# Performance work log

Measured on AMD Instinct MI355X. Metric: run time of the kernel, lower is better.

The kernel has to match this reference:

```python
import jax, jax.numpy as jnp
import numpy as np

LR, HR, H, D1 = 512, 2048, 4, 200
N = 2 * HR            # 4096 nodes (fully connected graph)
C1 = D1 // H          # 50  per-head dim, layer 1
C2 = HR // H          # 512 per-head dim, layer 2
EPS = 1e-5


def setup_inputs() -> dict:
    key = jax.random.key(0)
    ks = jax.random.split(key, 24)
    lin = lambda k, fi, fo: jax.random.normal(k, (fi, fo), jnp.float32) * 0.02
    vec = lambda k, d: jax.random.normal(k, (d,), jnp.float32) * 0.02
    inp = {"lr_x": jax.random.normal(ks[0], (LR, N), jnp.float32)}
    # TransformerConv 1: lr -> 200 (query/key/value/skip linears, each with bias)
    inp["Wq1"], inp["bq1"] = lin(ks[1], LR, D1), vec(ks[2], D1)
    inp["Wk1"], inp["bk1"] = lin(ks[3], LR, D1), vec(ks[4], D1)
    inp["Wv1"], inp["bv1"] = lin(ks[5], LR, D1), vec(ks[6], D1)
    inp["Ws1"], inp["bs1"] = lin(ks[7], LR, D1), vec(ks[8], D1)
    # GraphNorm 1
    inp["gn1_w"] = 1.0 + 0.1 * jax.random.normal(ks[9], (D1,), jnp.float32)
    inp["gn1_b"] = vec(ks[10], D1)
    inp["gn1_ms"] = 1.0 + 0.1 * jax.random.normal(ks[11], (D1,), jnp.float32)
    # TransformerConv 2: 200 -> 2048
    inp["Wq2"], inp["bq2"] = lin(ks[12], D1, HR), vec(ks[13], HR)
    inp["Wk2"], inp["bk2"] = lin(ks[14], D1, HR), vec(ks[15], HR)
    inp["Wv2"], inp["bv2"] = lin(ks[16], D1, HR), vec(ks[17], HR)
    inp["Ws2"], inp["bs2"] = lin(ks[18], D1, HR), vec(ks[19], HR)
    # GraphNorm 2
    inp["gn2_w"] = 1.0 + 0.1 * jax.random.normal(ks[20], (HR,), jnp.float32)
    inp["gn2_b"] = vec(ks[21], HR)
    inp["gn2_ms"] = 1.0 + 0.1 * jax.random.normal(ks[22], (HR,), jnp.float32)
    return inp


def _transformer_conv(x, Wq, bq, Wk, bk, Wv, bv, Ws, bs, heads, ch):
    # PyG TransformerConv on a fully-connected edge_index == dense multi-head attention
    n = x.shape[0]
    q = (x @ Wq + bq).reshape(n, heads, ch)
    k = (x @ Wk + bk).reshape(n, heads, ch)
    v = (x @ Wv + bv).reshape(n, heads, ch)
    scores = jnp.einsum('ihc,jhc->hij', q, k) / (ch ** 0.5)  # [H, N, N]
    attn = jax.nn.softmax(scores, axis=-1)                   # softmax over source nodes j
    out = jnp.einsum('hij,jhc->ihc', attn, v).reshape(n, heads * ch)
    return out + x @ Ws + bs                                 # root/skip connection


def _graph_norm(x, w, b, ms):
    # PyG GraphNorm: y = w * (x - ms*mean) / sqrt(E[(x - ms*mean)^2] + eps) + b
    mean = jnp.mean(x, axis=0, keepdims=True)
    out = x - mean * ms
    var = jnp.mean(out * out, axis=0, keepdims=True)
    return out * jax.lax.rsqrt(var + EPS) * w + b


def reference(lr_x, Wq1, bq1, Wk1, bk1, Wv1, bv1, Ws1, bs1, gn1_w, gn1_b, gn1_ms,
              Wq2, bq2, Wk2, bk2, Wv2, bv2, Ws2, bs2, gn2_w, gn2_b, gn2_ms):
    h = _transformer_conv(lr_x.T, Wq1, bq1, Wk1, bk1, Wv1, bv1, Ws1, bs1, H, C1)  # [N, 200]
    h = _graph_norm(h, gn1_w, gn1_b, gn1_ms)
    h2 = _transformer_conv(h, Wq2, bq2, Wk2, bk2, Wv2, bv2, Ws2, bs2, H, C2)      # [N, HR]
    h2 = _graph_norm(h2, gn2_w, gn2_b, gn2_ms).T                                  # [HR, N]
    h2 = h2 / jnp.linalg.norm(h2, axis=1, keepdims=True)
    return jax.nn.relu(h2 @ h2.T)                                                 # [HR, HR]
```

## Files before the change

### kernel.cpp

```cpp
#include <hip/hip_runtime.h>
#include <math.h>

typedef unsigned int u32;
typedef unsigned short ushort_t;
typedef __attribute__((ext_vector_type(8))) short short8;
typedef __attribute__((ext_vector_type(4))) float f32x4;

__device__ __forceinline__ ushort_t f2bf(float x) {
  u32 u = __float_as_uint(x);
  u32 r = (u + 0x7fffu + ((u >> 16) & 1u)) >> 16;
  return (ushort_t)r;
}
__device__ __forceinline__ float bf2f(u32 s) {
  return __uint_as_float(s << 16);
}
__device__ __forceinline__ void ld4bf(const ushort_t* p, float* o) {
  uint2 u = *(const uint2*)p;
  o[0] = bf2f(u.x & 0xffffu); o[1] = bf2f(u.x >> 16);
  o[2] = bf2f(u.y & 0xffffu); o[3] = bf2f(u.y >> 16);
}

__device__ __forceinline__ float block_sum256(float v, float* red) {
  #pragma unroll
  for (int o = 32; o > 0; o >>= 1) v += __shfl_down(v, o, 64);
  __syncthreads();
  if ((threadIdx.x & 63) == 0) red[threadIdx.x >> 6] = v;
  __syncthreads();
  return red[0] + red[1] + red[2] + red[3];
}

__global__ __launch_bounds__(512) void fused_attn1(
    const ushort_t* __restrict__ qk, const ushort_t* __restrict__ v,
    float* __restrict__ oP, float* __restrict__ r1p, float scale)
{
  __shared__ ushort_t Kl[2][4096];
  __shared__ ushort_t Vl[2][4096];
  __shared__ ushort_t Pl[128][80];
  const int t = threadIdx.x;
  const int lane = t & 63;
  const int wv = t >> 6;
  const int h = blockIdx.y;
  const int m0 = blockIdx.x * 128;
  const int z = blockIdx.z;
  const int lr = lane & 15;
  const int hk = lane >> 4;

  short8 aq0, aq1;
  {
    const ushort_t* qrow = qk + (size_t)(m0 + wv * 16 + lr) * 512 + h * 64;
    aq0 = *(const short8*)(qrow + hk * 8);
    aq1 = *(const short8*)(qrow + 32 + hk * 8);
  }

  f32x4 oAcc[4];
  #pragma unroll
  for (int i = 0; i < 4; ++i) oAcc[i] = (f32x4){0.f, 0.f, 0.f, 0.f};
  float racc[4] = {0.f, 0.f, 0.f, 0.f};

  const size_t kbase = (size_t)256 + h * 64;
  const int rS = t >> 3;
  const int cS = t & 7;
  const int lcS = cS ^ (rS & 7);

  {
    const int n0 = z * 16 * 64;
    __builtin_amdgcn_global_load_lds(
        (const __attribute__((address_space(1))) u32*)(qk + (size_t)(n0 + rS) * 512 + kbase + lcS * 8),
        (__attribute__((address_space(3))) u32*)(&Kl[0][t * 8]), 16, 0, 0);
    __builtin_amdgcn_global_load_lds(
        (const __attribute__((address_space(1))) u32*)(v + (size_t)(h * 128 + rS) * 4096 + n0 + lcS * 8),
        (__attribute__((address_space(3))) u32*)(&Vl[0][t * 8]), 16, 0, 0);
  }
  __syncthreads();

  int cur = 0;
  for (int it = 0; it < 16; ++it) {
    if (it + 1 < 16) {
      const int n1 = (z * 16 + it + 1) * 64;
      __builtin_amdgcn_global_load_lds(
          (const __attribute__((address_space(1))) u32*)(qk + (size_t)(n1 + rS) * 512 + kbase + lcS * 8),
          (__attribute__((address_space(3))) u32*)(&Kl[cur ^ 1][t * 8]), 16, 0, 0);
      __builtin_amdgcn_global_load_lds(
          (const __attribute__((address_space(1))) u32*)(v + (size_t)(h * 128 + rS) * 4096 + n1 + lcS * 8),
          (__attribute__((address_space(3))) u32*)(&Vl[cur ^ 1][t * 8]), 16, 0, 0);
    }
    f32x4 sA[4];
    #pragma unroll
    for (int nf = 0; nf < 4; ++nf) {
      const int rl = nf * 16 + lr;
      const char* kb = (const char*)&Kl[cur][0] + rl * 128;
      short8 b0 = *(const short8*)(kb + ((hk ^ (rl & 7)) * 16));
      short8 b1 = *(const short8*)(kb + (((4 + hk) ^ (rl & 7)) * 16));
      f32x4 sa = (f32x4){0.f, 0.f, 0.f, 0.f};
      sa = __builtin_amdgcn_mfma_f32_16x16x32_bf16(aq0, b0, sa, 0, 0, 0);
      sa = __builtin_amdgcn_mfma_f32_16x16x32_bf16(aq1, b1, sa, 0, 0, 0);
      sA[nf] = sa;
    }
    #pragma unroll
    for (int nf = 0; nf < 4; ++nf) {
      #pragma unroll
      for (int r = 0; r < 4; ++r) {
        float e = exp2f(sA[nf][r] * scale);
        racc[r] += e;
        Pl[wv * 16 + hk * 4 + r][nf * 16 + lr] = f2bf(e);
      }
    }
    short8 ap0 = *(const short8*)&Pl[wv * 16 + lr][hk * 8];
    short8 ap1 = *(const short8*)&Pl[wv * 16 + lr][32 + hk * 8];
    #pragma unroll
    for (int ff = 0; ff < 4; ++ff) {
      const int rl = ff * 16 + lr;
      const char* vb = (const char*)&Vl[cur][0] + rl * 128;
      short8 b0 = *(const short8*)(vb + ((hk ^ (rl & 7)) * 16));
      short8 b1 = *(const short8*)(vb + (((4 + hk) ^ (rl & 7)) * 16));
      oAcc[ff] = __builtin_amdgcn_mfma_f32_16x16x32_bf16(ap0, b0, oAcc[ff], 0, 0, 0);
      oAcc[ff] = __builtin_amdgcn_mfma_f32_16x16x32_bf16(ap1, b1, oAcc[ff], 0, 0, 0);
    }
    __syncthreads();
    cur ^= 1;
  }

  #pragma unroll
  for (int r = 0; r < 4; ++r) {
    racc[r] += __shfl_xor(racc[r], 1);
    racc[r] += __shfl_xor(racc[r], 2);
    racc[r] += __shfl_xor(racc[r], 4);
    racc[r] += __shfl_xor(racc[r], 8);
  }
  if (lr == 0) {
    float* rp = r1p + ((size_t)z * 4 + h) * 4096;
    #pragma unroll
    for (int r = 0; r < 4; ++r) rp[m0 + wv * 16 + hk * 4 + r] = racc[r];
  }
  float* ob = oP + (size_t)z * 512 * 4096;
  #pragma unroll
  for (int ff = 0; ff < 4; ++ff) {
    const size_t fbase = (size_t)(h * 128 + ff * 16 + lr) * 4096;
    #pragma unroll
    for (int r = 0; r < 4; ++r) {
      const int q = m0 + wv * 16 + hk * 4 + r;
      ob[fbase + q] = oAcc[ff][r];
    }
  }
}

__global__ __launch_bounds__(512, 2) void fused_attn2(
    const ushort_t* __restrict__ Tm, const ushort_t* __restrict__ X,
    const ushort_t* __restrict__ Xt, ushort_t* __restrict__ Up, float scale)
{
  __shared__ ushort_t Xl[16384];
  __shared__ ushort_t Xtl[2][16384];
  __shared__ ushort_t Pl[256][66];
  const int t = threadIdx.x;
  const int lane = t & 63;
  const int wv = t >> 6;
  const int h = blockIdx.y;
  const int m0 = blockIdx.x * 256;
  const int z = blockIdx.z;
  const int lr = lane & 15;
  const int hk = lane >> 4;

  short8 tq[2][7];
  #pragma unroll
  for (int qb = 0; qb < 2; ++qb) {
    const ushort_t* trow = Tm + ((size_t)h * 4096 + m0 + wv * 32 + qb * 16 + lr) * 256;
    #pragma unroll
    for (int s = 0; s < 7; ++s) tq[qb][s] = *(const short8*)(trow + s * 32 + hk * 8);
  }

  f32x4 uAcc[14][2];
  #pragma unroll
  for (int i = 0; i < 14; ++i) {
    uAcc[i][0] = (f32x4){0.f, 0.f, 0.f, 0.f};
    uAcc[i][1] = (f32x4){0.f, 0.f, 0.f, 0.f};
  }

  auto stageX = [&](int n0) {
    #pragma unroll
    for (int i = 0; i < 4; ++i) {
      const int st = t + i * 512;
      const int row = st >> 5, ph = st & 31;
      const int lc = (ph & 24) | ((ph & 7) ^ (row & 7));
      __builtin_amdgcn_global_load_lds(
          (const __attribute__((address_space(1))) u32*)(X + (size_t)(n0 + row) * 256 + lc * 8),
          (__attribute__((address_space(3))) u32*)(&Xl[st * 8]), 16, 0, 0);
    }
  };
  auto stageXt = [&](int buf, int n0) {
    #pragma unroll
    for (int i = 0; i < 4; ++i) {
      const int st = t + i * 512;
      const int row = st >> 3, ph = st & 7;
      const int lc = ph ^ (row & 7);
      __builtin_amdgcn_global_load_lds(
          (const __attribute__((address_space(1))) u32*)(Xt + (size_t)row * 4096 + n0 + lc * 8),
          (__attribute__((address_space(3))) u32*)(&Xtl[buf][st * 8]), 16, 0, 0);
    }
  };

  const int base = z * 16;
  stageX(base * 64);
  stageXt(0, base * 64);
  __syncthreads();

  int cur = 0;
  for (int it = 0; it < 16; ++it) {
    if (it + 1 < 16) stageXt(cur ^ 1, (base + it + 1) * 64);
    const char* xb = (const char*)&Xl[0];
    #pragma unroll
    for (int nf = 0; nf < 4; ++nf) {
      const int row = nf * 16 + lr;
      const char* rb = xb + row * 512;
      f32x4 sa0 = (f32x4){0.f, 0.f, 0.f, 0.f};
      f32x4 sa1 = (f32x4){0.f, 0.f, 0.f, 0.f};
      #pragma unroll
      for (int s = 0; s < 7; ++s) {
        const int c = s * 4 + hk;
        const int ph = (c & 24) | ((c & 7) ^ (row & 7));
        short8 xf = *(const short8*)(rb + ph * 16);
        sa0 = __builtin_amdgcn_mfma_f32_16x16x32_bf16(xf, tq[0][s], sa0, 0, 0, 0);
        sa1 = __builtin_amdgcn_mfma_f32_16x16x32_bf16(xf, tq[1][s], sa1, 0, 0, 0);
      }
      #pragma unroll
      for (int r = 0; r < 4; ++r) {
        Pl[wv * 32 + lr][nf * 16 + hk * 4 + r]      = f2bf(exp2f(sa0[r] * scale));
        Pl[wv * 32 + 16 + lr][nf * 16 + hk * 4 + r] = f2bf(exp2f(sa1[r] * scale));
      }
    }
    __syncthreads();
    if (it + 1 < 16) stageX((base + it + 1) * 64);
    short8 p00 = *(const short8*)((const char*)&Pl[wv * 32 + lr][0] + hk * 16);
    short8 p01 = *(const short8*)((const char*)&Pl[wv * 32 + lr][0] + (4 + hk) * 16);
    short8 p10 = *(const short8*)((const char*)&Pl[wv * 32 + 16 + lr][0] + hk * 16);
    short8 p11 = *(const short8*)((const char*)&Pl[wv * 32 + 16 + lr][0] + (4 + hk) * 16);
    const char* xtb = (const char*)&Xtl[cur][0];
    #pragma unroll
    for (int ff = 0; ff < 14; ++ff) {
      const int row = ff * 16 + lr;
      const char* rb2 = xtb + row * 128;
      short8 x0 = *(const short8*)(rb2 + ((hk ^ (row & 7)) * 16));
      short8 x1 = *(const short8*)(rb2 + (((4 + hk) ^ (row & 7)) * 16));
      uAcc[ff][0] = __builtin_amdgcn_mfma_f32_16x16x32_bf16(x0, p00, uAcc[ff][0], 0, 0, 0);
      uAcc[ff][0] = __builtin_amdgcn_mfma_f32_16x16x32_bf16(x1, p01, uAcc[ff][0], 0, 0, 0);
      uAcc[ff][1] = __builtin_amdgcn_mfma_f32_16x16x32_bf16(x0, p10, uAcc[ff][1], 0, 0, 0);
      uAcc[ff][1] = __builtin_amdgcn_mfma_f32_16x16x32_bf16(x1, p11, uAcc[ff][1], 0, 0, 0);
    }
    __syncthreads();
    cur ^= 1;
  }

  ushort_t* ub = Up + (size_t)(z * 4 + h) * 256 * 4096;
  #pragma unroll
  for (int ff = 0; ff < 14; ++ff) {
    #pragma unroll
    for (int qb = 0; qb < 2; ++qb) {
      #pragma unroll
      for (int r = 0; r < 4; ++r) {
        const int a = ff * 16 + hk * 4 + r;
        ub[(size_t)a * 4096 + m0 + wv * 32 + qb * 16 + lr] = f2bf(uAcc[ff][qb][r]);
      }
    }
  }
}

__global__ __launch_bounds__(256) void combine_u(
    const ushort_t* __restrict__ Up, ushort_t* __restrict__ Usum,
    float* __restrict__ r2)
{
  __shared__ float tl[64][65];
  const int t = threadIdx.x;
  const int qt = blockIdx.x;
  const int at = blockIdx.y;
  const int h  = blockIdx.z;
  const int c = t & 63;
  const int rb = t >> 6;
  const size_t PLN = (size_t)4 * 256 * 4096;
  #pragma unroll
  for (int i = 0; i < 16; ++i) {
    const int r = rb + i * 4;
    const int a = at * 64 + r;
    const int q = qt * 64 + c;
    const size_t i0 = ((size_t)h * 256 + a) * 4096 + q;
    float val = bf2f(Up[i0]) + bf2f(Up[PLN + i0])
              + bf2f(Up[2 * PLN + i0]) + bf2f(Up[3 * PLN + i0]);
    tl[r][c] = val;
    if (a == 200) r2[(size_t)h * 4096 + q] = val;
  }
  __syncthreads();
  #pragma unroll
  for (int i = 0; i < 16; ++i) {
    const int r = rb + i * 4;
    const int q = qt * 64 + r;
    const int a = at * 64 + c;
    Usum[((size_t)h * 4096 + q) * 256 + a] = f2bf(tl[c][r]);
  }
}

#define RD_A(bb, mm, cc) (*(const short8*)(lsAc + (bb)*32768 + arow + (mm)*2048 + (cc)))
#define RD_B(bb, nn, cc) (*(const short8*)(lsBc + (bb)*32768 + brow + (nn)*2048 + (cc)))

#define MM8(nn, bv) { \
  acc[0][nn] = __builtin_amdgcn_mfma_f32_16x16x32_bf16(a0, bv, acc[0][nn], 0,0,0); \
  acc[1][nn] = __builtin_amdgcn_mfma_f32_16x16x32_bf16(a1, bv, acc[1][nn], 0,0,0); \
  acc[2][nn] = __builtin_amdgcn_mfma_f32_16x16x32_bf16(a2, bv, acc[2][nn], 0,0,0); \
  acc[3][nn] = __builtin_amdgcn_mfma_f32_16x16x32_bf16(a3, bv, acc[3][nn], 0,0,0); \
  acc[4][nn] = __builtin_amdgcn_mfma_f32_16x16x32_bf16(a4, bv, acc[4][nn], 0,0,0); \
  acc[5][nn] = __builtin_amdgcn_mfma_f32_16x16x32_bf16(a5, bv, acc[5][nn], 0,0,0); \
  acc[6][nn] = __builtin_amdgcn_mfma_f32_16x16x32_bf16(a6, bv, acc[6][nn], 0,0,0); \
  acc[7][nn] = __builtin_amdgcn_mfma_f32_16x16x32_bf16(a7, bv, acc[7][nn], 0,0,0); }

#define STG(BASE, LD, LS, bb, hf, tt) { \
  _Pragma("unroll") \
  for (int ii = 0; ii < 2; ++ii) { \
    const int s_ = t + ii * 512; \
    const int r_ = s_ >> 3; \
    const int lc_ = (s_ & 7) ^ (r_ & 7); \
    __builtin_amdgcn_global_load_lds( \
      (const __attribute__((address_space(1))) u32*)((BASE) + (size_t)((hf) * 128 + r_) * (LD) + (size_t)(tt) * 64 + lc_ * 8), \
      (__attribute__((address_space(3))) u32*)(&(LS)[bb][(hf) * 8192 + s_ * 8]), 16, 0, 0); \
  } }

#define BAR() __builtin_amdgcn_s_barrier()
#define PRIO(x) __builtin_amdgcn_s_setprio(x)

#define GRP(bf, tS1, tS2) { \
  a0=RD_A(bf,0,c0); a1=RD_A(bf,1,c0); a2=RD_A(bf,2,c0); a3=RD_A(bf,3,c0); \
  a4=RD_A(bf,4,c0); a5=RD_A(bf,5,c0); a6=RD_A(bf,6,c0); a7=RD_A(bf,7,c0); \
  b0=RD_B(bf,0,c0); b1=RD_B(bf,1,c0); \
  STG(Ab, lda, lsA, 1-(bf), 1, tS1); STG(Bb, ldb, lsB, 1-(bf), 0, tS1); \
  BAR(); PRIO(1); MM8(0, b0); MM8(1, b1); PRIO(0); BAR(); \
  b2=RD_B(bf,2,c0); b3=RD_B(bf,3,c0); \
  STG(Bb, ldb, lsB, 1-(bf), 1, tS1); \
  BAR(); PRIO(1); MM8(2, b2); MM8(3, b3); PRIO(0); BAR(); \
  a0=RD_A(bf,0,c1); a1=RD_A(bf,1,c1); a2=RD_A(bf,2,c1); a3=RD_A(bf,3,c1); \
  a4=RD_A(bf,4,c1); a5=RD_A(bf,5,c1); a6=RD_A(bf,6,c1); a7=RD_A(bf,7,c1); \
  b0=RD_B(bf,0,c1); b1=RD_B(bf,1,c1); \
  BAR(); PRIO(1); MM8(0, b0); MM8(1, b1); PRIO(0); BAR(); \
  b2=RD_B(bf,2,c1); b3=RD_B(bf,3,c1); \
  STG(Ab, lda, lsA, (bf), 0, tS2); \
  BAR(); PRIO(1); MM8(2, b2); MM8(3, b3); PRIO(0); \
  asm volatile("s_waitcnt vmcnt(2)" ::: "memory"); \
  BAR(); }

template<int CMODE, bool RELU>
__global__ __launch_bounds__(512, 2) void mfma256_8ph(
    const ushort_t* __restrict__ A, const ushort_t* __restrict__ B,
    void* __restrict__ Cv, int lda, int ldb, int ldc,
    int K, int zsplit, size_t zA, size_t zB, size_t zC,
    int bShift, size_t bHead, int Mvalid, float scale)
{
  __shared__ ushort_t lsA[2][16384];
  __shared__ ushort_t lsB[2][16384];
  const int t = threadIdx.x;
  const int gx = gridDim.x;
  const int nwg = gx * gridDim.y;
  const int bid = blockIdx.y * gx + blockIdx.x;
  const int qq = nwg >> 3, rr_ = nwg & 7;
  const int xcd = bid & 7, idx = bid >> 3;
  const int swz = (xcd < rr_ ? xcd * (qq + 1) : rr_ * (qq + 1) + (xcd - rr_) * qq) + idx;
  const int m0 = (swz / gx) * 256;
  const int n0 = (swz % gx) * 256;
  const int z = blockIdx.z;
  int Kc = K, kOff = 0;
  size_t aZ = 0, bZ = 0, cZ = 0;
  if (zsplit > 1) { Kc = K / zsplit; kOff = z * Kc; cZ = (size_t)z * zC; }
  else { aZ = (size_t)z * zA; bZ = (size_t)z * zB; cZ = (size_t)z * zC; }
  const ushort_t* Ab = A + aZ + (size_t)m0 * lda + kOff;
  const ushort_t* Bb = B + bZ + (size_t)n0 * ldb + kOff
                     + (bShift >= 0 ? (size_t)(m0 >> bShift) * bHead : 0);
  const int NT = Kc / 64;

  f32x4 acc[8][4];
  #pragma unroll
  for (int i = 0; i < 8; ++i)
    #pragma unroll
    for (int j = 0; j < 4; ++j) acc[i][j] = (f32x4){0.f, 0.f, 0.f, 0.f};

  const int lane = t & 63;
  const int wv = t >> 6;
  const int wr = (wv >> 2) * 128;
  const int wc = (wv & 3) * 64;
  const int lr = lane & 15;
  const int kc = lane >> 4;
  const int sw = lane & 7;
  const int c0 = (kc ^ sw) * 16;
  const int c1 = c0 ^ 64;
  const int arow = (wr + lr) * 128;
  const int brow = (wc + lr) * 128;
  const char* lsAc = (const char*)lsA;
  const char* lsBc = (const char*)lsB;

  short8 a0, a1, a2, a3, a4, a5, a6, a7, b0, b1, b2, b3;

  STG(Ab, lda, lsA, 0, 0, 0); STG(Ab, lda, lsA, 0, 1, 0);
  STG(Bb, ldb, lsB, 0, 0, 0); STG(Bb, ldb, lsB, 0, 1, 0);
  STG(Ab, lda, lsA, 1, 0, 1);
  asm volatile("s_waitcnt vmcnt(2)" ::: "memory");
  BAR();

  const int NITER = NT >> 1;
  for (int it = 0; it < NITER; ++it) {
    const int tb = 2 * it;
    const int s1 = tb + 1;
    const int s2 = (tb + 2 < NT) ? tb + 2 : 0;
    const int s3 = (tb + 3 < NT) ? tb + 3 : 0;
    GRP(0, s1, s2)
    GRP(1, s2, s3)
  }

  const int row4 = (lane >> 4) * 4;
  const int coln = lane & 15;
  float* Cf = (float*)Cv + cZ;
  ushort_t* Ch = (ushort_t*)Cv + cZ;
  #pragma unroll
  for (int m = 0; m < 8; ++m) {
    #pragma unroll
    for (int r = 0; r < 4; ++r) {
      const int gm = m0 + wr + m * 16 + row4 + r;
      const bool ok = gm < Mvalid;
      #pragma unroll
      for (int n = 0; n < 4; ++n) {
        const int gn = n0 + wc + n * 16 + coln;
        float v = acc[m][n][r] * scale;
        if (RELU) v = fmaxf(v, 0.f);
        if (ok) {
          if (CMODE == 0)      Cf[(size_t)gm * ldc + gn] = v;
          else if (CMODE == 1) Ch[(size_t)gm * ldc + gn] = f2bf(v);
          else                 atomicAdd(&Cf[(size_t)gm * ldc + gn], v);
        }
      }
    }
  }
}

#undef GRP
#undef STG
#undef MM8
#undef RD_A
#undef RD_B

template<int CMODE, bool RELU>
__global__ __launch_bounds__(256) void mfma_bt(
    const ushort_t* __restrict__ A, const ushort_t* __restrict__ B,
    void* __restrict__ Cv, int lda, int ldb, int ldc,
    int K, int Ksplit, size_t zA, size_t zB, size_t zC,
    int bShift, size_t bHead, int mMask, int Mvalid, float scale)
{
  __shared__ ushort_t lsA[2][128 * 32];
  __shared__ ushort_t lsB[2][128 * 32];
  const int t  = threadIdx.x;
  const int m0 = blockIdx.y * 128;
  const int n0 = blockIdx.x * 128;
  const int z = blockIdx.z;
  int Kc = K, kOff = 0;
  size_t aZ = 0, bZ = 0, cZ = 0;
  if (Ksplit > 1) { Kc = K / Ksplit; kOff = z * Kc; cZ = (size_t)z * zC; }
  else { aZ = (size_t)z * zA; bZ = (size_t)z * zB; cZ = (size_t)z * zC; }
  const int NT = Kc / 32;
  const ushort_t* Ab = A + aZ + (size_t)m0 * lda + kOff;
  const ushort_t* Bb = B + bZ + (size_t)n0 * ldb + kOff
                     + (bShift >= 0 ? (size_t)(m0 >> bShift) * bHead : 0);
  const int cs = t & 3;

  f32x4 acc[4][4];
  #pragma unroll
  for (int i = 0; i < 4; ++i)
    #pragma unroll
    for (int j = 0; j < 4; ++j) acc[i][j] = (f32x4){0.f, 0.f, 0.f, 0.f};

  const int lane = t & 63;
  const int wv = t >> 6;
  const int wr = (wv >> 1) * 64;
  const int wc = (wv & 1) * 64;
  const int lr = lane & 15;
  const int kc = lane >> 4;

  int roffA[4], roffB[4];
  #pragma unroll
  for (int m = 0; m < 4; ++m) {
    int ra = wr + m * 16 + lr;
    roffA[m] = ra * 64 + ((kc ^ (ra & 3)) * 16);
    int rb = wc + m * 16 + lr;
    roffB[m] = rb * 64 + ((kc ^ (rb & 3)) * 16);
  }

  auto stage = [&](int buf, int kt) {
    const ushort_t* As = Ab + kt * 32;
    const ushort_t* Bs = Bb + kt * 32;
    #pragma unroll
    for (int i = 0; i < 2; ++i) {
      int s = t + i * 256;
      int r = s >> 2;
      int c = cs ^ (r & 3);
      __builtin_amdgcn_global_load_lds(
          (const __attribute__((address_space(1))) u32*)(As + (size_t)r * lda + c * 8),
          (__attribute__((address_space(3))) u32*)(&lsA[buf][s * 8]), 16, 0, 0);
    }
    #pragma unroll
    for (int i = 0; i < 2; ++i) {
      int s = t + i * 256;
      int r = s >> 2;
      int c = cs ^ (r & 3);
      __builtin_amdgcn_global_load_lds(
          (const __attribute__((address_space(1))) u32*)(Bs + (size_t)r * ldb + c * 8),
          (__attribute__((address_space(3))) u32*)(&lsB[buf][s * 8]), 16, 0, 0);
    }
  };

  stage(0, 0);
  __syncthreads();
  int cur = 0;
  for (int kt = 0; kt < NT; ++kt) {
    if (kt + 1 < NT) stage(cur ^ 1, kt + 1);
    short8 af[4], bfr[4];
    const char* baseA = (const char*)&lsA[cur][0];
    const char* baseB = (const char*)&lsB[cur][0];
    #pragma unroll
    for (int m = 0; m < 4; ++m) af[m]  = *(const short8*)(baseA + roffA[m]);
    #pragma unroll
    for (int n = 0; n < 4; ++n) bfr[n] = *(const short8*)(baseB + roffB[n]);
    #pragma unroll
    for (int m = 0; m < 4; ++m)
      #pragma unroll
      for (int n = 0; n < 4; ++n)
        acc[m][n] = __builtin_amdgcn_mfma_f32_16x16x32_bf16(af[m], bfr[n], acc[m][n], 0, 0, 0);
    __syncthreads();
    cur ^= 1;
  }

  const int row4 = (lane >> 4) * 4;
  const int coln = lane & 15;
  float* Cf = (float*)Cv + cZ;
  ushort_t* Ch = (ushort_t*)Cv + cZ;
  #pragma unroll
  for (int m = 0; m < 4; ++m) {
    #pragma unroll
    for (int r = 0; r < 4; ++r) {
      const int gm = m0 + wr + m * 16 + row4 + r;
      const bool ok = (mMask >= 0) ? ((gm & mMask) < Mvalid) : (gm < Mvalid);
      #pragma unroll
      for (int n = 0; n < 4; ++n) {
        const int gn = n0 + wc + n * 16 + coln;
        float v = acc[m][n][r] * scale;
        if (RELU) v = fmaxf(v, 0.f);
        if (ok) {
          if (CMODE == 0)      Cf[(size_t)gm * ldc + gn] = v;
          else if (CMODE == 1) Ch[(size_t)gm * ldc + gn] = f2bf(v);
          else                 atomicAdd(&Cf[(size_t)gm * ldc + gn], v);
        }
      }
    }
  }
}

__global__ __launch_bounds__(256) void wt_conv(
    const float* __restrict__ W, const float* __restrict__ bias,
    ushort_t* __restrict__ dst, int Mtot, int ldw, int Kv, int Kp,
    int PADH, int VALH)
{
  const int m = blockIdx.x;
  const int h = m / PADH, c0 = m % PADH;
  const int fout = h * VALH + c0;
  const bool valid = (c0 < VALH) && (fout < Mtot);
  for (int k = threadIdx.x; k < Kp; k += blockDim.x) {
    float v = 0.f;
    if (valid) {
      if (k < Kv) v = W[(size_t)k * ldw + fout];
      else if (k == Kv) v = bias[fout];
    }
    dst[(size_t)m * Kp + k] = f2bf(v);
  }
}

__global__ __launch_bounds__(256) void wt_trans(
    const float* __restrict__ W, const float* __restrict__ bias,
    ushort_t* __restrict__ dst)
{
  const int rid = blockIdx.x;
  const int h = rid >> 8, a = rid & 255;
  for (int f = threadIdx.x; f < 512; f += 256) {
    float v = 0.f;
    if (a < 200)       v = W[(size_t)a * 2048 + h * 512 + f];
    else if (a == 200) v = bias[h * 512 + f];
    dst[(size_t)rid * 512 + f] = f2bf(v);
  }
}

__global__ __launch_bounds__(256) void xt_conv(
    const float* __restrict__ h1nT, ushort_t* __restrict__ Xt)
{
  const int a = blockIdx.x;
  for (int q = threadIdx.x; q < 4096; q += 256) {
    float v = (a < 200) ? h1nT[(size_t)a * 4096 + q] : ((a == 200) ? 1.f : 0.f);
    Xt[(size_t)a * 4096 + q] = f2bf(v);
  }
}

__global__ __launch_bounds__(256) void trans_pad(
    const float* __restrict__ src, ushort_t* __restrict__ dst, int Kv, int Kp)
{
  __shared__ float tl[64][65];
  const int t = threadIdx.x;
  const int f0 = blockIdx.x * 64;
  const int i0 = blockIdx.y * 64;
  const int c = t & 63, rbase = t >> 6;
  #pragma unroll
  for (int it = 0; it < 16; ++it) {
    int r = rbase + it * 4;
    int f = f0 + r;
    tl[r][c] = (f < Kv) ? src[(size_t)f * 4096 + i0 + c] : 0.f;
  }
  __syncthreads();
  #pragma unroll
  for (int it = 0; it < 16; ++it) {
    int r = rbase + it * 4;
    int f = f0 + c;
    if (f < Kp) {
      float v = (f < Kv) ? tl[c][r] : ((f == Kv) ? 1.f : 0.f);
      dst[(size_t)(i0 + r) * Kp + f] = f2bf(v);
    }
  }
}

__global__ __launch_bounds__(256) void graph_norm_attn1(
    const ushort_t* __restrict__ skip, const float* __restrict__ oP,
    const float* __restrict__ r1p, float* __restrict__ out,
    const float* __restrict__ w, const float* __restrict__ b,
    const float* __restrict__ ms)
{
  __shared__ float red[4];
  const int t = threadIdx.x;
  const int row = blockIdx.x;
  const int h = row / 50;
  const int pr = h * 128 + row % 50;
  const ushort_t* sk = skip + (size_t)pr * 4096;
  const size_t OSTR = (size_t)512 * 4096;
  float v[16];
  float s = 0.f;
  #pragma unroll
  for (int e = 0; e < 4; ++e) {
    const int idx = t * 4 + 1024 * e;
    float a[4];
    ld4bf(&sk[idx], a);
    float4 o0 = *(const float4*)&oP[(size_t)pr * 4096 + idx];
    float4 o1 = *(const float4*)&oP[OSTR + (size_t)pr * 4096 + idx];
    float4 o2 = *(const float4*)&oP[2 * OSTR + (size_t)pr * 4096 + idx];
    float4 o3 = *(const float4*)&oP[3 * OSTR + (size_t)pr * 4096 + idx];
    float4 r0 = *(const float4*)&r1p[(size_t)h * 4096 + idx];
    float4 r1 = *(const float4*)&r1p[(size_t)(4 + h) * 4096 + idx];
    float4 r2 = *(const float4*)&r1p[(size_t)(8 + h) * 4096 + idx];
    float4 r3 = *(const float4*)&r1p[(size_t)(12 + h) * 4096 + idx];
    v[e*4+0] = a[0] + (o0.x + o1.x + o2.x + o3.x) / (r0.x + r1.x + r2.x + r3.x);
    v[e*4+1] = a[1] + (o0.y + o1.y + o2.y + o3.y) / (r0.y + r1.y + r2.y + r3.y);
    v[e*4+2] = a[2] + (o0.z + o1.z + o2.z + o3.z) / (r0.z + r1.z + r2.z + r3.z);
    v[e*4+3] = a[3] + (o0.w + o1.w + o2.w + o3.w) / (r0.w + r1.w + r2.w + r3.w);
    s += v[e*4+0] + v[e*4+1] + v[e*4+2] + v[e*4+3];
  }
  const float mean = block_sum256(s, red) * (1.f / 4096.f);
  const float sub = mean * ms[row];
  float s2 = 0.f;
  #pragma unroll
  for (int e = 0; e < 16; ++e) { v[e] -= sub; s2 += v[e] * v[e]; }
  const float var = block_sum256(s2, red) * (1.f / 4096.f);
  const float scl = rsqrtf(var + 1e-5f) * w[row];
  const float bb = b[row];
  float* y = out + (size_t)row * 4096;
  #pragma unroll
  for (int e = 0; e < 4; ++e) {
    float o0[4];
    #pragma unroll
    for (int q = 0; q < 4; ++q) o0[q] = v[e * 4 + q] * scl + bb;
    *(float4*)&y[t * 4 + 1024 * e] = *(float4*)&o0[0];
  }
}

__global__ __launch_bounds__(256) void graph_norm_attn2(
    const ushort_t* __restrict__ skip, const ushort_t* __restrict__ O,
    const float* __restrict__ r2, ushort_t* __restrict__ out,
    const float* __restrict__ w, const float* __restrict__ b,
    const float* __restrict__ ms)
{
  __shared__ float red[4];
  const int t = threadIdx.x;
  const int row = blockIdx.x;
  const ushort_t* sk = skip + (size_t)row * 4096;
  const ushort_t* pa = O + (size_t)row * 4096;
  const float* rr = r2 + (size_t)(row >> 9) * 4096;
  float v[16];
  float s = 0.f;
  #pragma unroll
  for (int e = 0; e < 4; ++e) {
    const int idx = t * 4 + 1024 * e;
    float a[4], oa[4];
    ld4bf(&sk[idx], a); ld4bf(&pa[idx], oa);
    float4 rv = *(const float4*)&rr[idx];
    v[e*4+0] = a[0] + oa[0] / rv.x;
    v[e*4+1] = a[1] + oa[1] / rv.y;
    v[e*4+2] = a[2] + oa[2] / rv.z;
    v[e*4+3] = a[3] + oa[3] / rv.w;
    s += v[e*4+0] + v[e*4+1] + v[e*4+2] + v[e*4+3];
  }
  const float mean = block_sum256(s, red) * (1.f / 4096.f);
  const float sub = mean * ms[row];
  float s2 = 0.f;
  #pragma unroll
  for (int e = 0; e < 16; ++e) { v[e] -= sub; s2 += v[e] * v[e]; }
  const float var = block_sum256(s2, red) * (1.f / 4096.f);
  const float scl = rsqrtf(var + 1e-5f) * w[row];
  const float bb = b[row];
  #pragma unroll
  for (int e = 0; e < 16; ++e) v[e] = v[e] * scl + bb;
  float s3 = 0.f;
  #pragma unroll
  for (int e = 0; e < 16; ++e) s3 += v[e] * v[e];
  const float osc = rsqrtf(block_sum256(s3, red));
  ushort_t* y = out + (size_t)row * 4096;
  #pragma unroll
  for (int e = 0; e < 4; ++e) {
    ushort_t o0[4];
    #pragma unroll
    for (int q = 0; q < 4; ++q) o0[q] = f2bf(v[e * 4 + q] * osc);
    *(ushort2*)&y[t * 4 + 1024 * e] = *(ushort2*)&o0[0];
    *(ushort2*)&y[t * 4 + 1024 * e + 2] = *(ushort2*)&o0[2];
  }
}

__global__ __launch_bounds__(256) void add4_relu_bf16(
    const ushort_t* __restrict__ g, float* __restrict__ out)
{
  const size_t i = (size_t)blockIdx.x * 256 + threadIdx.x;
  const size_t ss = (size_t)2048 * 2048;
  float a[4], b[4], c[4], d[4];
  ld4bf(&g[i * 4], a);
  ld4bf(&g[ss + i * 4], b);
  ld4bf(&g[2 * ss + i * 4], c);
  ld4bf(&g[3 * ss + i * 4], d);
  float4 o;
  o.x = fmaxf(a[0] + b[0] + c[0] + d[0], 0.f);
  o.y = fmaxf(a[1] + b[1] + c[1] + d[1], 0.f);
  o.z = fmaxf(a[2] + b[2] + c[2] + d[2], 0.f);
  o.w = fmaxf(a[3] + b[3] + c[3] + d[3], 0.f);
  ((float4*)out)[i] = o;
}

extern "C" void kernel_launch(void* const* d_in, const int* in_sizes, int n_in,
                              void* d_out, int out_size, void* d_ws, size_t ws_size,
                              hipStream_t stream)
{
  (void)in_sizes; (void)n_in; (void)out_size; (void)ws_size;
  const float* lr_x = (const float*)d_in[0];
  const float* Wq1 = (const float*)d_in[1];  const float* bq1 = (const float*)d_in[2];
  const float* Wk1 = (const float*)d_in[3];  const float* bk1 = (const float*)d_in[4];
  const float* Wv1 = (const float*)d_in[5];  const float* bv1 = (const float*)d_in[6];
  const float* Ws1 = (const float*)d_in[7];  const float* bs1 = (const float*)d_in[8];
  const float* gn1w = (const float*)d_in[9]; const float* gn1b = (const float*)d_in[10];
  const float* gn1ms = (const float*)d_in[11];
  const float* Wq2 = (const float*)d_in[12]; const float* bq2 = (const float*)d_in[13];
  const float* Wk2 = (const float*)d_in[14]; const float* bk2 = (const float*)d_in[15];
  const float* Wv2 = (const float*)d_in[16]; const float* bv2 = (const float*)d_in[17];
  const float* Ws2 = (const float*)d_in[18]; const float* bs2 = (const float*)d_in[19];
  const float* gn2w = (const float*)d_in[20]; const float* gn2b = (const float*)d_in[21];
  const float* gn2ms = (const float*)d_in[22];

  char* p = (char*)d_ws;
  auto alloc = [&](size_t bytes) { char* r = p; p += (bytes + 255) & ~(size_t)255; return r; };
  char*     scrA = alloc((size_t)32 * 1024 * 1024);
  ushort_t* xb   = (ushort_t*)alloc((size_t)4096 * 544 * 2);
  ushort_t* qk1b = (ushort_t*)alloc((size_t)4096 * 512 * 2);
  ushort_t* v1s  = (ushort_t*)alloc((size_t)1024 * 4096 * 2);
  char*     u0   = alloc((size_t)16 * 1024 * 1024);
  float*    h1nT = (float*)   alloc((size_t)200 * 4096 * 4);
  ushort_t* h1nb = (ushort_t*)alloc((size_t)4096 * 256 * 2);
  ushort_t* Wqk1 = (ushort_t*)alloc((size_t)512 * 544 * 2);
  ushort_t* Wvs1 = (ushort_t*)alloc((size_t)1024 * 544 * 2);
  ushort_t* Wcat = (ushort_t*)alloc((size_t)4096 * 256 * 2);
  ushort_t* Qt   = (ushort_t*)alloc((size_t)4 * 256 * 512 * 2);
  ushort_t* Kt   = (ushort_t*)alloc((size_t)4 * 256 * 512 * 2);
  ushort_t* Mtall= (ushort_t*)alloc((size_t)4 * 256 * 256 * 2);
  ushort_t* Tall = (ushort_t*)alloc((size_t)4 * 4096 * 256 * 2);
  ushort_t* Xtb  = (ushort_t*)alloc((size_t)256 * 4096 * 2);
  ushort_t* vs2b = (ushort_t*)alloc((size_t)4096 * 4096 * 2);
  ushort_t* Usum = (ushort_t*)alloc((size_t)4 * 4096 * 256 * 2);
  ushort_t* Opl  = (ushort_t*)alloc((size_t)2048 * 4096 * 2);
  float*    r1p  = (float*)   alloc((size_t)16 * 4096 * 4);
  float*    r2   = (float*)   alloc((size_t)4 * 4096 * 4);
  float*    oP   = (float*)scrA;
  ushort_t* UpH  = (ushort_t*)scrA;
  ushort_t* g4   = (ushort_t*)scrA;
  ushort_t* h2b  = (ushort_t*)u0;

  const dim3 b256(256, 1, 1);
  const dim3 b512(512, 1, 1);
  const float LOG2E = 1.4426950408889634f;
  const float sc1e = 0.14142135623730951f * LOG2E;
  const float sc2e = 0.04419417382415922f * LOG2E;

  wt_conv<<<dim3(256),  b256, 0, stream>>>(Wq1, bq1, Wqk1,             200, 200, 512, 544, 64, 50);
  wt_conv<<<dim3(256),  b256, 0, stream>>>(Wk1, bk1, Wqk1 + 256 * 544, 200, 200, 512, 544, 64, 50);
  wt_conv<<<dim3(512),  b256, 0, stream>>>(Wv1, bv1, Wvs1,             200, 200, 512, 544, 128, 50);
  wt_conv<<<dim3(512),  b256, 0, stream>>>(Ws1, bs1, Wvs1 + 512 * 544, 200, 200, 512, 544, 128, 50);
  wt_conv<<<dim3(2048), b256, 0, stream>>>(Wv2, bv2, Wcat,              2048, 2048, 200, 256, 2048, 2048);
  wt_conv<<<dim3(2048), b256, 0, stream>>>(Ws2, bs2, Wcat + 2048 * 256, 2048, 2048, 200, 256, 2048, 2048);
  wt_trans<<<dim3(1024), b256, 0, stream>>>(Wq2, bq2, Qt);
  wt_trans<<<dim3(1024), b256, 0, stream>>>(Wk2, bk2, Kt);
  trans_pad<<<dim3(9, 64), b256, 0, stream>>>(lr_x, xb, 512, 544);

  mfma_bt<1, false><<<dim3(4, 32), b256, 0, stream>>>(
      xb, Wqk1, qk1b, 544, 544, 512, 544, 1, 0, 0, 0, -1, 0, -1, 4096, 1.f);
  mfma_bt<1, false><<<dim3(32, 8), b256, 0, stream>>>(
      Wvs1, xb, v1s, 544, 544, 4096, 544, 1, 0, 0, 0, -1, 0, -1, 1024, 1.f);

  fused_attn1<<<dim3(32, 4, 4), b512, 0, stream>>>(qk1b, v1s, oP, r1p, sc1e);
  graph_norm_attn1<<<dim3(200), b256, 0, stream>>>(
      v1s + (size_t)512 * 4096, oP, r1p, h1nT, gn1w, gn1b, gn1ms);
  trans_pad<<<dim3(4, 64), b256, 0, stream>>>(h1nT, h1nb, 200, 256);
  xt_conv<<<dim3(256), b256, 0, stream>>>(h1nT, Xtb);

  mfma_bt<1, false><<<dim3(32, 32), b256, 0, stream>>>(
      Wcat, h1nb, vs2b, 256, 256, 4096, 224, 1, 0, 0, 0, -1, 0, -1, 4096, 1.f);

  mfma_bt<1, false><<<dim3(2, 2, 4), b256, 0, stream>>>(
      Kt, Qt, Mtall, 512, 512, 256, 512, 1,
      (size_t)256 * 512, (size_t)256 * 512, (size_t)256 * 256, -1, 0, -1, 256, 1.f);
  mfma_bt<1, false><<<dim3(2, 32, 4), b256, 0, stream>>>(
      h1nb, Mtall, Tall, 256, 256, 256, 224, 1,
      0, (size_t)256 * 256, (size_t)4096 * 256, -1, 0, -1, 4096, 1.f);
  fused_attn2<<<dim3(16, 4, 4), b512, 0, stream>>>(Tall, h1nb, Xtb, UpH, sc2e);
  combine_u<<<dim3(64, 4, 4), b256, 0, stream>>>(UpH, Usum, r2);
  mfma_bt<1, false><<<dim3(32, 16), b256, 0, stream>>>(
      Wcat, Usum, Opl, 256, 256, 4096, 224, 1,
      0, 0, 0, 9, (size_t)4096 * 256, -1, 2048, 1.f);
  graph_norm_attn2<<<dim3(2048), b256, 0, stream>>>(
      vs2b + (size_t)2048 * 4096, Opl, r2, h2b, gn2w, gn2b, gn2ms);

  mfma256_8ph<1, false><<<dim3(8, 8, 4), b512, 0, stream>>>(
      h2b, h2b, g4, 4096, 4096, 2048, 4096, 4,
      0, 0, (size_t)2048 * 2048, -1, 0, 2048, 1.f);
  add4_relu_bf16<<<dim3(4096), b256, 0, stream>>>(g4, (float*)d_out);
}
```

Baseline: 328.1 us.

## Give each wave two query tiles in attn1 and vectorize P stores in attn2

fused_attn1 now runs 256 threads per block, with each wave handling 32 query rows (two 16-row tiles) instead of 16. Each K/V fragment read from LDS therefore feeds twice as many MFMAs, and staging is done in two passes per thread. In fused_attn2 the P tile row pitch goes from 66 to 72 elements, and the four bf16 values per fragment are packed into a single 8-byte LDS store instead of four scalar stores. The mfma_bt K-tile count now rounds up. In exchange, attn1 uses more registers per thread and has fewer waves per block to hide latency.

```diff
diff --git a/kernel.cpp b/kernel.cpp
--- a/kernel.cpp
+++ b/kernel.cpp
@@ -29,7 +29,7 @@
   return red[0] + red[1] + red[2] + red[3];
 }
 
-__global__ __launch_bounds__(512) void fused_attn1(
+__global__ __launch_bounds__(256) void fused_attn1(
     const ushort_t* __restrict__ qk, const ushort_t* __restrict__ v,
     float* __restrict__ oP, float* __restrict__ r1p, float scale)
 {
@@ -45,102 +45,113 @@
   const int lr = lane & 15;
   const int hk = lane >> 4;
 
-  short8 aq0, aq1;
-  {
-    const ushort_t* qrow = qk + (size_t)(m0 + wv * 16 + lr) * 512 + h * 64;
-    aq0 = *(const short8*)(qrow + hk * 8);
-    aq1 = *(const short8*)(qrow + 32 + hk * 8);
-  }
-
-  f32x4 oAcc[4];
-  #pragma unroll
-  for (int i = 0; i < 4; ++i) oAcc[i] = (f32x4){0.f, 0.f, 0.f, 0.f};
-  float racc[4] = {0.f, 0.f, 0.f, 0.f};
+  short8 aq[2][2];
+  #pragma unroll
+  for (int qb = 0; qb < 2; ++qb) {
+    const ushort_t* qrow = qk + (size_t)(m0 + wv * 32 + qb * 16 + lr) * 512 + h * 64;
+    aq[qb][0] = *(const short8*)(qrow + hk * 8);
+    aq[qb][1] = *(const short8*)(qrow + 32 + hk * 8);
+  }
+
+  f32x4 oAcc[4][2];
+  #pragma unroll
+  for (int i = 0; i < 4; ++i) {
+    oAcc[i][0] = (f32x4){0.f, 0.f, 0.f, 0.f};
+    oAcc[i][1] = (f32x4){0.f, 0.f, 0.f, 0.f};
+  }
+  float racc[2][4] = {{0.f,0.f,0.f,0.f},{0.f,0.f,0.f,0.f}};
 
   const size_t kbase = (size_t)256 + h * 64;
-  const int rS = t >> 3;
-  const int cS = t & 7;
-  const int lcS = cS ^ (rS & 7);
-
-  {
-    const int n0 = z * 16 * 64;
-    __builtin_amdgcn_global_load_lds(
-        (const __attribute__((address_space(1))) u32*)(qk + (size_t)(n0 + rS) * 512 + kbase + lcS * 8),
-        (__attribute__((address_space(3))) u32*)(&Kl[0][t * 8]), 16, 0, 0);
-    __builtin_amdgcn_global_load_lds(
-        (const __attribute__((address_space(1))) u32*)(v + (size_t)(h * 128 + rS) * 4096 + n0 + lcS * 8),
-        (__attribute__((address_space(3))) u32*)(&Vl[0][t * 8]), 16, 0, 0);
-  }
+
+  auto stage = [&](int buf, int n0) {
+    #pragma unroll
+    for (int i = 0; i < 2; ++i) {
+      const int st = t + i * 256;
+      const int row = st >> 3, cS = st & 7;
+      const int lc = cS ^ (row & 7);
+      __builtin_amdgcn_global_load_lds(
+          (const __attribute__((address_space(1))) u32*)(qk + (size_t)(n0 + row) * 512 + kbase + lc * 8),
+          (__attribute__((address_space(3))) u32*)(&Kl[buf][st * 8]), 16, 0, 0);
+      __builtin_amdgcn_global_load_lds(
+          (const __attribute__((address_space(1))) u32*)(v + (size_t)(h * 128 + row) * 4096 + n0 + lc * 8),
+          (__attribute__((address_space(3))) u32*)(&Vl[buf][st * 8]), 16, 0, 0);
+    }
+  };
+
+  stage(0, z * 1024);
   __syncthreads();
 
   int cur = 0;
   for (int it = 0; it < 16; ++it) {
-    if (it + 1 < 16) {
-      const int n1 = (z * 16 + it + 1) * 64;
-      __builtin_amdgcn_global_load_lds(
-          (const __attribute__((address_space(1))) u32*)(qk + (size_t)(n1 + rS) * 512 + kbase + lcS * 8),
-          (__attribute__((address_space(3))) u32*)(&Kl[cur ^ 1][t * 8]), 16, 0, 0);
-      __builtin_amdgcn_global_load_lds(
-          (const __attribute__((address_space(1))) u32*)(v + (size_t)(h * 128 + rS) * 4096 + n1 + lcS * 8),
-          (__attribute__((address_space(3))) u32*)(&Vl[cur ^ 1][t * 8]), 16, 0, 0);
-    }
-    f32x4 sA[4];
+    if (it + 1 < 16) stage(cur ^ 1, z * 1024 + (it + 1) * 64);
     #pragma unroll
     for (int nf = 0; nf < 4; ++nf) {
       const int rl = nf * 16 + lr;
       const char* kb = (const char*)&Kl[cur][0] + rl * 128;
       short8 b0 = *(const short8*)(kb + ((hk ^ (rl & 7)) * 16));
       short8 b1 = *(const short8*)(kb + (((4 + hk) ^ (rl & 7)) * 16));
-      f32x4 sa = (f32x4){0.f, 0.f, 0.f, 0.f};
-      sa = __builtin_amdgcn_mfma_f32_16x16x32_bf16(aq0, b0, sa, 0, 0, 0);
-      sa = __builtin_amdgcn_mfma_f32_16x16x32_bf16(aq1, b1, sa, 0, 0, 0);
-      sA[nf] = sa;
-    }
-    #pragma unroll
-    for (int nf = 0; nf < 4; ++nf) {
       #pragma unroll
-      for (int r = 0; r < 4; ++r) {
-        float e = exp2f(sA[nf][r] * scale);
-        racc[r] += e;
-        Pl[wv * 16 + hk * 4 + r][nf * 16 + lr] = f2bf(e);
+      for (int qb = 0; qb < 2; ++qb) {
+        f32x4 sa = (f32x4){0.f, 0.f, 0.f, 0.f};
+        sa = __builtin_amdgcn_mfma_f32_16x16x32_bf16(aq[qb][0], b0, sa, 0, 0, 0);
+        sa = __builtin_amdgcn_mfma_f32_16x16x32_bf16(aq[qb][1], b1, sa, 0, 0, 0);
+        #pragma unroll
+        for (int r = 0; r < 4; ++r) {
+          float e = exp2f(sa[r] * scale);
+          racc[qb][r] += e;
+          Pl[wv * 32 + qb * 16 + hk * 4 + r][nf * 16 + lr] = f2bf(e);
+        }
       }
     }
-    short8 ap0 = *(const short8*)&Pl[wv * 16 + lr][hk * 8];
-    short8 ap1 = *(const short8*)&Pl[wv * 16 + lr][32 + hk * 8];
+    short8 ap[2][2];
+    #pragma unroll
+    for (int qb = 0; qb < 2; ++qb) {
+      ap[qb][0] = *(const short8*)&Pl[wv * 32 + qb * 16 + lr][hk * 8];
+      ap[qb][1] = *(const short8*)&Pl[wv * 32 + qb * 16 + lr][32 + hk * 8];
+    }
     #pragma unroll
     for (int ff = 0; ff < 4; ++ff) {
       const int rl = ff * 16 + lr;
       const char* vb = (const char*)&Vl[cur][0] + rl * 128;
       short8 b0 = *(const short8*)(vb + ((hk ^ (rl & 7)) * 16));
       short8 b1 = *(const short8*)(vb + (((4 + hk) ^ (rl & 7)) * 16));
-      oAcc[ff] = __builtin_amdgcn_mfma_f32_16x16x32_bf16(ap0, b0, oAcc[ff], 0, 0, 0);
-      oAcc[ff] = __builtin_amdgcn_mfma_f32_16x16x32_bf16(ap1, b1, oAcc[ff], 0, 0, 0);
+      #pragma unroll
+      for (int qb = 0; qb < 2; ++qb) {
+        oAcc[ff][qb] = __builtin_amdgcn_mfma_f32_16x16x32_bf16(ap[qb][0], b0, oAcc[ff][qb], 0, 0, 0);
+        oAcc[ff][qb] = __builtin_amdgcn_mfma_f32_16x16x32_bf16(ap[qb][1], b1, oAcc[ff][qb], 0, 0, 0);
+      }
     }
     __syncthreads();
     cur ^= 1;
   }
 
   #pragma unroll
-  for (int r = 0; r < 4; ++r) {
-    racc[r] += __shfl_xor(racc[r], 1);
-    racc[r] += __shfl_xor(racc[r], 2);
-    racc[r] += __shfl_xor(racc[r], 4);
-    racc[r] += __shfl_xor(racc[r], 8);
+  for (int qb = 0; qb < 2; ++qb) {
+    #pragma unroll
+    for (int r = 0; r < 4; ++r) {
+      racc[qb][r] += __shfl_xor(racc[qb][r], 1);
+      racc[qb][r] += __shfl_xor(racc[qb][r], 2);
+      racc[qb][r] += __shfl_xor(racc[qb][r], 4);
+      racc[qb][r] += __shfl_xor(racc[qb][r], 8);
+    }
   }
   if (lr == 0) {
     float* rp = r1p + ((size_t)z * 4 + h) * 4096;
     #pragma unroll
-    for (int r = 0; r < 4; ++r) rp[m0 + wv * 16 + hk * 4 + r] = racc[r];
+    for (int qb = 0; qb < 2; ++qb)
+      #pragma unroll
+      for (int r = 0; r < 4; ++r)
+        rp[m0 + wv * 32 + qb * 16 + hk * 4 + r] = racc[qb][r];
   }
   float* ob = oP + (size_t)z * 512 * 4096;
   #pragma unroll
   for (int ff = 0; ff < 4; ++ff) {
     const size_t fbase = (size_t)(h * 128 + ff * 16 + lr) * 4096;
     #pragma unroll
-    for (int r = 0; r < 4; ++r) {
-      const int q = m0 + wv * 16 + hk * 4 + r;
-      ob[fbase + q] = oAcc[ff][r];
-    }
+    for (int qb = 0; qb < 2; ++qb)
+      #pragma unroll
+      for (int r = 0; r < 4; ++r)
+        ob[fbase + m0 + wv * 32 + qb * 16 + hk * 4 + r] = oAcc[ff][qb][r];
   }
 }
 
@@ -150,7 +161,7 @@
 {
   __shared__ ushort_t Xl[16384];
   __shared__ ushort_t Xtl[2][16384];
-  __shared__ ushort_t Pl[256][66];
+  __shared__ ushort_t Pl[256][72];
   const int t = threadIdx.x;
   const int lane = t & 63;
   const int wv = t >> 6;
@@ -221,11 +232,13 @@
         sa0 = __builtin_amdgcn_mfma_f32_16x16x32_bf16(xf, tq[0][s], sa0, 0, 0, 0);
         sa1 = __builtin_amdgcn_mfma_f32_16x16x32_bf16(xf, tq[1][s], sa1, 0, 0, 0);
       }
-      #pragma unroll
-      for (int r = 0; r < 4; ++r) {
-        Pl[wv * 32 + lr][nf * 16 + hk * 4 + r]      = f2bf(exp2f(sa0[r] * scale));
-        Pl[wv * 32 + 16 + lr][nf * 16 + hk * 4 + r] = f2bf(exp2f(sa1[r] * scale));
-      }
+      uint2 w0, w1;
+      w0.x = (u32)f2bf(exp2f(sa0[0] * scale)) | ((u32)f2bf(exp2f(sa0[1] * scale)) << 16);
+      w0.y = (u32)f2bf(exp2f(sa0[2] * scale)) | ((u32)f2bf(exp2f(sa0[3] * scale)) << 16);
+      w1.x = (u32)f2bf(exp2f(sa1[0] * scale)) | ((u32)f2bf(exp2f(sa1[1] * scale)) << 16);
+      w1.y = (u32)f2bf(exp2f(sa1[2] * scale)) | ((u32)f2bf(exp2f(sa1[3] * scale)) << 16);
+      *(uint2*)((char*)&Pl[wv * 32 + lr][0] + nf * 32 + hk * 8) = w0;
+      *(uint2*)((char*)&Pl[wv * 32 + 16 + lr][0] + nf * 32 + hk * 8) = w1;
     }
     __syncthreads();
     if (it + 1 < 16) stageX((base + it + 1) * 64);
@@ -456,7 +469,7 @@
   size_t aZ = 0, bZ = 0, cZ = 0;
   if (Ksplit > 1) { Kc = K / Ksplit; kOff = z * Kc; cZ = (size_t)z * zC; }
   else { aZ = (size_t)z * zA; bZ = (size_t)z * zB; cZ = (size_t)z * zC; }
-  const int NT = Kc / 32;
+  const int NT = (Kc + 31) / 32;
   const ushort_t* Ab = A + aZ + (size_t)m0 * lda + kOff;
   const ushort_t* Bb = B + bZ + (size_t)n0 * ldb + kOff
                      + (bShift >= 0 ? (size_t)(m0 >> bShift) * bHead : 0);
@@ -810,7 +823,7 @@
   mfma_bt<1, false><<<dim3(32, 8), b256, 0, stream>>>(
       Wvs1, xb, v1s, 544, 544, 4096, 544, 1, 0, 0, 0, -1, 0, -1, 1024, 1.f);
 
-  fused_attn1<<<dim3(32, 4, 4), b512, 0, stream>>>(qk1b, v1s, oP, r1p, sc1e);
+  fused_attn1<<<dim3(32, 4, 4), b256, 0, stream>>>(qk1b, v1s, oP, r1p, sc1e);
   graph_norm_attn1<<<dim3(200), b256, 0, stream>>>(
       v1s + (size_t)512 * 4096, oP, r1p, h1nT, gn1w, gn1b, gn1ms);
   trans_pad<<<dim3(4, 64), b256, 0, stream>>>(h1nT, h1nb, 200, 256);
```

Measured after the change: 327.1 us. Within noise of the previous version (-0.3%).
